# Kernel tuning notes

Measured on AMD Instinct MI355X. Metric: run time of the kernel, lower is better.

The kernel has to match this reference:

```python
import jax, jax.numpy as jnp
import numpy as np

N_HEAD = 16
D_HEAD = 64
D_MODEL = 1024
SCALE = 1.0 / D_HEAD ** 0.5


def setup_inputs() -> dict:
    key = jax.random.key(0)
    k1, k2 = jax.random.split(key)
    h = jax.random.normal(k1, (2048, 2, D_MODEL), dtype=jnp.float32)
    # torch Linear weight layout: [out_features, in_features]
    w_qkv = jax.random.normal(k2, (3 * N_HEAD * D_HEAD, D_MODEL), dtype=jnp.float32) * (D_MODEL ** -0.5)
    return {"h": h, "w_qkv": w_qkv}


def reference(h, w_qkv):
    qlen, bsz, _ = h.shape
    heads = h @ w_qkv.T  # [qlen, bsz, 3*n_head*d_head]
    head_q, head_k, head_v = jnp.split(heads, 3, axis=-1)
    head_q = head_q.reshape(qlen, bsz, N_HEAD, D_HEAD)
    head_k = head_k.reshape(qlen, bsz, N_HEAD, D_HEAD)
    head_v = head_v.reshape(qlen, bsz, N_HEAD, D_HEAD)
    attn_score = jnp.einsum('ibnd,jbnd->ijbn', head_q, head_k) * SCALE
    attn_prob = jax.nn.softmax(attn_score, axis=1)  # softmax over key dim j
    # dropout is identity at p=0.0 / eval mode
    attn_vec = jnp.einsum('ijbn,jbnd->ibnd', attn_prob, head_v)
    attn_vec = attn_vec.reshape(qlen, bsz, N_HEAD * D_HEAD)
    return attn_vec, attn_prob
```

## Files before the change

### kernel.cpp

```cpp
#include <hip/hip_runtime.h>

typedef _Float16 f16;
typedef f16 f16x8 __attribute__((ext_vector_type(8)));
typedef f16 f16x4 __attribute__((ext_vector_type(4)));
typedef float f32x4 __attribute__((ext_vector_type(4)));

#define QLEN 2048
#define BSZ 2
#define NH 16
#define DH 64
#define DM 1024
#define NBN (BSZ*NH)
#define SCALE 0.125f

static __device__ __forceinline__ f32x4 mfma16(f16x8 a, f16x8 b, f32x4 c) {
  return __builtin_amdgcn_mfma_f32_16x16x32_f16(a, b, c, 0, 0, 0);
}

static __device__ __forceinline__ void gload_lds16(const void* g, void* l) {
  __builtin_amdgcn_global_load_lds((const __attribute__((address_space(1))) unsigned int*)g,
                                   (__attribute__((address_space(3))) unsigned int*)l,
                                   16, 0, 0);
}

__global__ __launch_bounds__(256) void cvt_f32_f16(const float* __restrict__ s,
                                                   f16* __restrict__ d, int n4) {
  int idx = blockIdx.x * 256 + threadIdx.x;
  if (idx >= n4) return;
  f32x4 v = ((const f32x4*)s)[idx];
  f16x4 o;
#pragma unroll
  for (int q = 0; q < 4; ++q) o[q] = (f16)v[q];
  ((f16x4*)d)[idx] = o;
}

__global__ __launch_bounds__(256) void qkv_gemm(const f16* __restrict__ A, const f16* __restrict__ W,
                                                f16* __restrict__ Qs, f16* __restrict__ Ks,
                                                f16* __restrict__ Vt) {
  __shared__ f16 As[128 * 32];
  __shared__ f16 Bs[128 * 32];
  const int bid = blockIdx.x;
  const int r0 = (bid & 31) << 7;
  const int c0 = (bid >> 5) << 7;
  const int t = threadIdx.x;
  const int lane = t & 63, w = t >> 6;
  const int wr = (w >> 1) << 6, wc = (w & 1) << 6;
  const int l15 = lane & 15, lhi = lane >> 4;

  f32x4 acc[4][4] = {};

  const f16* ga = A + (size_t)(r0 + (t >> 2)) * DM + ((t & 3) << 3);
  const f16* gb = W + (size_t)(c0 + (t >> 2)) * DM + ((t & 3) << 3);
  char* la = (char*)As + w * 1024;
  char* lb = (char*)Bs + w * 1024;

  for (int k0 = 0; k0 < DM; k0 += 32) {
    __syncthreads();
    gload_lds16(ga + k0, la);
    gload_lds16(ga + k0 + (size_t)64 * DM, la + 4096);
    gload_lds16(gb + k0, lb);
    gload_lds16(gb + k0 + (size_t)64 * DM, lb + 4096);
    __syncthreads();
    f16x8 af[4], bf[4];
#pragma unroll
    for (int m = 0; m < 4; ++m)
      af[m] = *(const f16x8*)&As[(wr + m * 16 + l15) * 32 + lhi * 8];
#pragma unroll
    for (int n = 0; n < 4; ++n)
      bf[n] = *(const f16x8*)&Bs[(wc + n * 16 + l15) * 32 + lhi * 8];
#pragma unroll
    for (int m = 0; m < 4; ++m)
#pragma unroll
      for (int n = 0; n < 4; ++n)
        acc[m][n] = mfma16(af[m], bf[n], acc[m][n]);
  }

  const int part = c0 >> 10;
#pragma unroll
  for (int m = 0; m < 4; ++m) {
#pragma unroll
    for (int n = 0; n < 4; ++n) {
#pragma unroll
      for (int q = 0; q < 4; ++q) {
        int r = r0 + wr + m * 16 + lhi * 4 + q;
        int c = c0 + wc + n * 16 + l15;
        int i = r >> 1, b = r & 1;
        int nh = (c >> 6) & 15, d = c & 63;
        int bn = b * 16 + nh;
        f16 v = (f16)acc[m][n][q];
        if (part == 0)       Qs[((size_t)bn * QLEN + i) * DH + d] = v;
        else if (part == 1)  Ks[((size_t)bn * QLEN + i) * DH + d] = v;
        else                 Vt[((size_t)bn * DH + d) * QLEN + i] = v;
      }
    }
  }
}

__global__ __launch_bounds__(256) void flash_attn(const f16* __restrict__ Qs, const f16* __restrict__ Ks,
                                                  const f16* __restrict__ Vt, float* __restrict__ av,
                                                  float* __restrict__ sm, float* __restrict__ srl) {
  __shared__ f16 plds[4][16 * 32];
  const int bid = blockIdx.x;
  const int bn = bid >> 4, ib = bid & 15;
  const int t = threadIdx.x, lane = t & 63, w = t >> 6;
  const int l15 = lane & 15, lhi = lane >> 4;
  const int i0 = (ib << 7) + (w << 5);
  const f16* Qb = Qs + ((size_t)bn << 17);
  const f16* Kb = Ks + ((size_t)bn << 17);
  const f16* Vb = Vt + ((size_t)bn << 17);
  f16* pw = plds[w];

  f16x8 qf[2][2];
#pragma unroll
  for (int rg = 0; rg < 2; ++rg)
#pragma unroll
    for (int kc = 0; kc < 2; ++kc)
      qf[rg][kc] = *(const f16x8*)&Qb[(size_t)(i0 + rg * 16 + l15) * DH + kc * 32 + lhi * 8];

  f32x4 o[2][4] = {};
  float mrun[2][4], lrun[2][4];
#pragma unroll
  for (int rg = 0; rg < 2; ++rg)
#pragma unroll
    for (int q = 0; q < 4; ++q) { mrun[rg][q] = -1e30f; lrun[rg][q] = 0.f; }

  for (int j0 = 0; j0 < QLEN; j0 += 32) {
    f16x8 kf[2][2], vf[4];
#pragma unroll
    for (int jc = 0; jc < 2; ++jc)
#pragma unroll
      for (int kc = 0; kc < 2; ++kc)
        kf[jc][kc] = *(const f16x8*)&Kb[(size_t)(j0 + jc * 16 + l15) * DH + kc * 32 + lhi * 8];
#pragma unroll
    for (int dc = 0; dc < 4; ++dc)
      vf[dc] = *(const f16x8*)&Vb[(size_t)(dc * 16 + l15) * QLEN + j0 + lhi * 8];

#pragma unroll
    for (int rg = 0; rg < 2; ++rg) {
      f32x4 s[2];
#pragma unroll
      for (int jc = 0; jc < 2; ++jc) {
        f32x4 z = {0.f, 0.f, 0.f, 0.f};
        z = mfma16(qf[rg][0], kf[jc][0], z);
        z = mfma16(qf[rg][1], kf[jc][1], z);
        s[jc] = z;
      }
      float p[2][4], alpha[4];
#pragma unroll
      for (int q = 0; q < 4; ++q) {
        float v0 = s[0][q] * SCALE, v1 = s[1][q] * SCALE;
        float tm = fmaxf(v0, v1);
        tm = fmaxf(tm, __shfl_xor(tm, 1));
        tm = fmaxf(tm, __shfl_xor(tm, 2));
        tm = fmaxf(tm, __shfl_xor(tm, 4));
        tm = fmaxf(tm, __shfl_xor(tm, 8));
        float mnew = fmaxf(mrun[rg][q], tm);
        alpha[q] = __expf(mrun[rg][q] - mnew);
        mrun[rg][q] = mnew;
        p[0][q] = __expf(v0 - mnew);
        p[1][q] = __expf(v1 - mnew);
        float r = p[0][q] + p[1][q];
        r += __shfl_xor(r, 1);
        r += __shfl_xor(r, 2);
        r += __shfl_xor(r, 4);
        r += __shfl_xor(r, 8);
        lrun[rg][q] = lrun[rg][q] * alpha[q] + r;
      }
#pragma unroll
      for (int dc = 0; dc < 4; ++dc)
#pragma unroll
        for (int q = 0; q < 4; ++q)
          o[rg][dc][q] *= alpha[q];
#pragma unroll
      for (int jc = 0; jc < 2; ++jc)
#pragma unroll
        for (int q = 0; q < 4; ++q)
          pw[(lhi * 4 + q) * 32 + jc * 16 + l15] = (f16)p[jc][q];
      f16x8 pa = *(const f16x8*)&pw[l15 * 32 + lhi * 8];
#pragma unroll
      for (int dc = 0; dc < 4; ++dc)
        o[rg][dc] = mfma16(pa, vf[dc], o[rg][dc]);
    }
  }

  const int b = bn >> 4, nh = bn & 15;
#pragma unroll
  for (int rg = 0; rg < 2; ++rg)
#pragma unroll
    for (int dc = 0; dc < 4; ++dc)
#pragma unroll
      for (int q = 0; q < 4; ++q) {
        int i = i0 + rg * 16 + lhi * 4 + q;
        av[((size_t)i * BSZ + b) * (NH * DH) + nh * DH + dc * 16 + l15] =
            o[rg][dc][q] / lrun[rg][q];
      }
  if (l15 == 0) {
#pragma unroll
    for (int rg = 0; rg < 2; ++rg)
#pragma unroll
      for (int q = 0; q < 4; ++q) {
        int i = i0 + rg * 16 + lhi * 4 + q;
        sm[bn * QLEN + i] = mrun[rg][q];
        srl[bn * QLEN + i] = 1.0f / lrun[rg][q];
      }
  }
}

__global__ __launch_bounds__(256, 2) void write_probs(const f16* __restrict__ Qs, const f16* __restrict__ Ks,
                                                      const float* __restrict__ sm, const float* __restrict__ srl,
                                                      float* __restrict__ pout) {
  __shared__ f16 tile[2][16 * 32 * 32];
  const int bid = blockIdx.x;
  const int it = bid >> 3, jt = bid & 7;
  const int i0 = it << 4, j0 = jt << 8;
  const int t = threadIdx.x, lane = t & 63, w = t >> 6;
  const int l15 = lane & 15, lhi = lane >> 4;

  float mm[8][4], rl[8][4];
#pragma unroll
  for (int bl = 0; bl < 8; ++bl) {
    const int bn = w * 8 + bl;
#pragma unroll
    for (int q = 0; q < 4; ++q) {
      const int i = i0 + lhi * 4 + q;
      mm[bl][q] = sm[bn * QLEN + i];
      rl[bl][q] = srl[bn * QLEN + i];
    }
  }

  const int o = t & 3;
  const int jl_s = (t >> 2) & 31;
  const int ihalf = t >> 7;
  const int quad = o ^ ((jl_s & 7) >> 1);
  const bool hsw = (jl_s & 1);

  for (int ch = 0; ch < 8; ++ch) {
    f16* tb = tile[ch & 1];
    const int jbase = j0 + ch * 32;

    f16 stv[8][2][4];
#pragma unroll
    for (int bl = 0; bl < 8; ++bl) {
      const int bn = w * 8 + bl;
      const f16* Qb = Qs + ((size_t)bn << 17);
      const f16* Kb = Ks + ((size_t)bn << 17);
      f16x8 qf[2], kf[2][2];
#pragma unroll
      for (int kc = 0; kc < 2; ++kc)
        qf[kc] = *(const f16x8*)&Qb[(size_t)(i0 + l15) * DH + kc * 32 + lhi * 8];
#pragma unroll
      for (int jc = 0; jc < 2; ++jc)
#pragma unroll
        for (int kc = 0; kc < 2; ++kc)
          kf[jc][kc] = *(const f16x8*)&Kb[(size_t)(jbase + jc * 16 + l15) * DH + kc * 32 + lhi * 8];
#pragma unroll
      for (int jc = 0; jc < 2; ++jc) {
        f32x4 z = {0.f, 0.f, 0.f, 0.f};
        z = mfma16(qf[0], kf[jc][0], z);
        z = mfma16(qf[1], kf[jc][1], z);
#pragma unroll
        for (int q = 0; q < 4; ++q)
          stv[bl][jc][q] = (f16)(__expf(z[q] * SCALE - mm[bl][q]) * rl[bl][q]);
      }
    }

#pragma unroll
    for (int h = 0; h < 2; ++h) {
      const int g = w * 2 + h;
#pragma unroll
      for (int jc = 0; jc < 2; ++jc)
#pragma unroll
        for (int q = 0; q < 4; ++q) {
          const int i_l = lhi * 4 + q;
          const int jl = jc * 16 + l15;
          f16x4 v = {stv[4 * h + 0][jc][q], stv[4 * h + 1][jc][q],
                     stv[4 * h + 2][jc][q], stv[4 * h + 3][jc][q]};
          *(f16x4*)&tb[(i_l * 32 + jl) * 32 + ((g ^ (jl & 7)) << 2)] = v;
        }
    }
    __syncthreads();

#pragma unroll
    for (int p = 0; p < 8; ++p) {
      const int i_l = p * 2 + ihalf;
      f16x8 v = *(const f16x8*)&tb[(i_l * 32 + jl_s) * 32 + (quad << 3)];
      f16x4 vl = {v[0], v[1], v[2], v[3]};
      f16x4 vh = {v[4], v[5], v[6], v[7]};
      f16x4 fa = hsw ? vh : vl;
      f16x4 fb = hsw ? vl : vh;
      f32x4 lo = {(float)fa[0], (float)fa[1], (float)fa[2], (float)fa[3]};
      f32x4 hi = {(float)fb[0], (float)fb[1], (float)fb[2], (float)fb[3]};
      float* op = pout + ((size_t)(i0 + i_l) * QLEN + jbase + jl_s) * NBN + o * 8;
      __builtin_nontemporal_store(lo, (f32x4*)op);
      __builtin_nontemporal_store(hi, (f32x4*)(op + 4));
    }
  }
}

extern "C" void kernel_launch(void* const* d_in, const int* in_sizes, int n_in,
                              void* d_out, int out_size, void* d_ws, size_t ws_size,
                              hipStream_t stream) {
  const float* h  = (const float*)d_in[0];
  const float* wq = (const float*)d_in[1];
  float* av   = (float*)d_out;
  float* pout = av + (size_t)QLEN * BSZ * NH * DH;

  char* ws = (char*)d_ws;
  f16* hh  = (f16*)ws;
  f16* wh  = (f16*)(ws + (8u << 20));
  f16* Qsc = (f16*)(ws + (16u << 20));
  f16* Ksc = (f16*)(ws + (24u << 20));
  f16* Vtc = (f16*)(ws + (32u << 20));
  float* smv  = (float*)(ws + (40u << 20));
  float* srlv = (float*)(ws + (40u << 20) + (QLEN * NBN * 4));

  const int nh4 = QLEN * BSZ * DM / 4;
  const int nw4 = 3 * NH * DH * DM / 4;
  cvt_f32_f16<<<nh4 / 256, 256, 0, stream>>>(h, hh, nh4);
  cvt_f32_f16<<<nw4 / 256, 256, 0, stream>>>(wq, wh, nw4);
  qkv_gemm<<<32 * 24, 256, 0, stream>>>(hh, wh, Qsc, Ksc, Vtc);
  flash_attn<<<NBN * 16, 256, 0, stream>>>(Qsc, Ksc, Vtc, av, smv, srlv);
  write_probs<<<128 * 8, 256, 0, stream>>>(Qsc, Ksc, smv, srlv, pout);
}
```

Measured before the change: 378.8 us.

## Widen write_probs key chunk to 64 with single LDS tile and reload softmax stats

```diff
diff --git a/kernel.cpp b/kernel.cpp
--- a/kernel.cpp
+++ b/kernel.cpp
@@ -209,88 +209,82 @@
 __global__ __launch_bounds__(256, 2) void write_probs(const f16* __restrict__ Qs, const f16* __restrict__ Ks,
                                                       const float* __restrict__ sm, const float* __restrict__ srl,
                                                       float* __restrict__ pout) {
-  __shared__ f16 tile[2][16 * 32 * 32];
+  __shared__ f16 tile[16 * 64 * 32];
   const int bid = blockIdx.x;
   const int it = bid >> 3, jt = bid & 7;
   const int i0 = it << 4, j0 = jt << 8;
   const int t = threadIdx.x, lane = t & 63, w = t >> 6;
   const int l15 = lane & 15, lhi = lane >> 4;
 
-  float mm[8][4], rl[8][4];
-#pragma unroll
-  for (int bl = 0; bl < 8; ++bl) {
-    const int bn = w * 8 + bl;
-#pragma unroll
-    for (int q = 0; q < 4; ++q) {
-      const int i = i0 + lhi * 4 + q;
-      mm[bl][q] = sm[bn * QLEN + i];
-      rl[bl][q] = srl[bn * QLEN + i];
-    }
-  }
-
   const int o = t & 3;
-  const int jl_s = (t >> 2) & 31;
-  const int ihalf = t >> 7;
-  const int quad = o ^ ((jl_s & 7) >> 1);
-  const bool hsw = (jl_s & 1);
-
-  for (int ch = 0; ch < 8; ++ch) {
-    f16* tb = tile[ch & 1];
-    const int jbase = j0 + ch * 32;
-
-    f16 stv[8][2][4];
+  const int j_s = t >> 2;
+  const int sp = o ^ ((j_s & 7) >> 1);
+  const bool hsw = (j_s & 1);
+
+  for (int sc = 0; sc < 4; ++sc) {
+    const int jbase = j0 + sc * 64;
+
+    f16x4 stv[8][4];
 #pragma unroll
     for (int bl = 0; bl < 8; ++bl) {
       const int bn = w * 8 + bl;
       const f16* Qb = Qs + ((size_t)bn << 17);
       const f16* Kb = Ks + ((size_t)bn << 17);
-      f16x8 qf[2], kf[2][2];
+      f16x8 qf[2], kf[4][2];
 #pragma unroll
       for (int kc = 0; kc < 2; ++kc)
         qf[kc] = *(const f16x8*)&Qb[(size_t)(i0 + l15) * DH + kc * 32 + lhi * 8];
 #pragma unroll
-      for (int jc = 0; jc < 2; ++jc)
+      for (int jc = 0; jc < 4; ++jc)
 #pragma unroll
         for (int kc = 0; kc < 2; ++kc)
           kf[jc][kc] = *(const f16x8*)&Kb[(size_t)(jbase + jc * 16 + l15) * DH + kc * 32 + lhi * 8];
-#pragma unroll
-      for (int jc = 0; jc < 2; ++jc) {
+      float mm[4], rl[4];
+#pragma unroll
+      for (int q = 0; q < 4; ++q) {
+        const int i = i0 + lhi * 4 + q;
+        mm[q] = sm[bn * QLEN + i];
+        rl[q] = srl[bn * QLEN + i];
+      }
+#pragma unroll
+      for (int jc = 0; jc < 4; ++jc) {
         f32x4 z = {0.f, 0.f, 0.f, 0.f};
         z = mfma16(qf[0], kf[jc][0], z);
         z = mfma16(qf[1], kf[jc][1], z);
 #pragma unroll
         for (int q = 0; q < 4; ++q)
-          stv[bl][jc][q] = (f16)(__expf(z[q] * SCALE - mm[bl][q]) * rl[bl][q]);
-      }
-    }
+          stv[bl][jc][q] = (f16)(__expf(z[q] * SCALE - mm[q]) * rl[q]);
+      }
+    }
+
+    __syncthreads();
 
 #pragma unroll
     for (int h = 0; h < 2; ++h) {
       const int g = w * 2 + h;
 #pragma unroll
-      for (int jc = 0; jc < 2; ++jc)
+      for (int jc = 0; jc < 4; ++jc)
 #pragma unroll
         for (int q = 0; q < 4; ++q) {
           const int i_l = lhi * 4 + q;
           const int jl = jc * 16 + l15;
           f16x4 v = {stv[4 * h + 0][jc][q], stv[4 * h + 1][jc][q],
                      stv[4 * h + 2][jc][q], stv[4 * h + 3][jc][q]};
-          *(f16x4*)&tb[(i_l * 32 + jl) * 32 + ((g ^ (jl & 7)) << 2)] = v;
+          *(f16x4*)&tile[(i_l * 64 + jl) * 32 + ((g ^ (jl & 7)) << 2)] = v;
         }
     }
     __syncthreads();
 
 #pragma unroll
-    for (int p = 0; p < 8; ++p) {
-      const int i_l = p * 2 + ihalf;
-      f16x8 v = *(const f16x8*)&tb[(i_l * 32 + jl_s) * 32 + (quad << 3)];
+    for (int r = 0; r < 16; ++r) {
+      f16x8 v = *(const f16x8*)&tile[(r * 64 + j_s) * 32 + (sp << 3)];
       f16x4 vl = {v[0], v[1], v[2], v[3]};
       f16x4 vh = {v[4], v[5], v[6], v[7]};
       f16x4 fa = hsw ? vh : vl;
       f16x4 fb = hsw ? vl : vh;
       f32x4 lo = {(float)fa[0], (float)fa[1], (float)fa[2], (float)fa[3]};
       f32x4 hi = {(float)fb[0], (float)fb[1], (float)fb[2], (float)fb[3]};
-      float* op = pout + ((size_t)(i0 + i_l) * QLEN + jbase + jl_s) * NBN + o * 8;
+      float* op = pout + ((size_t)(i0 + r) * QLEN + jbase + j_s) * NBN + o * 8;
       __builtin_nontemporal_store(lo, (f32x4*)op);
       __builtin_nontemporal_store(hi, (f32x4*)(op + 4));
     }
```

After: 432.6 us. 14.2% more time.

## Widen QKV GEMM K-tile, swizzle LDS, and stage epilogue through LDS

Applied to the files above, without the earlier changes.

```diff
diff --git a/kernel.cpp b/kernel.cpp
--- a/kernel.cpp
+++ b/kernel.cpp
@@ -37,8 +37,9 @@
 __global__ __launch_bounds__(256) void qkv_gemm(const f16* __restrict__ A, const f16* __restrict__ W,
                                                 f16* __restrict__ Qs, f16* __restrict__ Ks,
                                                 f16* __restrict__ Vt) {
-  __shared__ f16 As[128 * 32];
-  __shared__ f16 Bs[128 * 32];
+  __shared__ f16 S[2][128 * 64];
+  f16* As = S[0];
+  f16* Bs = S[1];
   const int bid = blockIdx.x;
   const int r0 = (bid & 31) << 7;
   const int c0 = (bid >> 5) << 7;
@@ -49,50 +50,75 @@
 
   f32x4 acc[4][4] = {};
 
-  const f16* ga = A + (size_t)(r0 + (t >> 2)) * DM + ((t & 3) << 3);
-  const f16* gb = W + (size_t)(c0 + (t >> 2)) * DM + ((t & 3) << 3);
+  const int scol = (((t & 7) ^ ((t >> 3) & 7)) << 3);
+  const f16* ga = A + (size_t)(r0 + (t >> 3)) * DM + scol;
+  const f16* gb = W + (size_t)(c0 + (t >> 3)) * DM + scol;
   char* la = (char*)As + w * 1024;
   char* lb = (char*)Bs + w * 1024;
 
-  for (int k0 = 0; k0 < DM; k0 += 32) {
+  for (int k0 = 0; k0 < DM; k0 += 64) {
     __syncthreads();
-    gload_lds16(ga + k0, la);
-    gload_lds16(ga + k0 + (size_t)64 * DM, la + 4096);
-    gload_lds16(gb + k0, lb);
-    gload_lds16(gb + k0 + (size_t)64 * DM, lb + 4096);
+#pragma unroll
+    for (int it = 0; it < 4; ++it) {
+      gload_lds16(ga + k0 + (size_t)(it * 32) * DM, la + it * 4096);
+      gload_lds16(gb + k0 + (size_t)(it * 32) * DM, lb + it * 4096);
+    }
     __syncthreads();
-    f16x8 af[4], bf[4];
-#pragma unroll
-    for (int m = 0; m < 4; ++m)
-      af[m] = *(const f16x8*)&As[(wr + m * 16 + l15) * 32 + lhi * 8];
+#pragma unroll
+    for (int kk = 0; kk < 2; ++kk) {
+      f16x8 af[4], bf[4];
+#pragma unroll
+      for (int m = 0; m < 4; ++m) {
+        const int r = wr + m * 16 + l15;
+        af[m] = *(const f16x8*)&As[r * 64 + (((kk * 4 + lhi) ^ (r & 7)) << 3)];
+      }
+#pragma unroll
+      for (int n = 0; n < 4; ++n) {
+        const int r = wc + n * 16 + l15;
+        bf[n] = *(const f16x8*)&Bs[r * 64 + (((kk * 4 + lhi) ^ (r & 7)) << 3)];
+      }
+#pragma unroll
+      for (int m = 0; m < 4; ++m)
+#pragma unroll
+        for (int n = 0; n < 4; ++n)
+          acc[m][n] = mfma16(af[m], bf[n], acc[m][n]);
+    }
+  }
+
+  const int part = c0 >> 10;
+  const int nh_base = (c0 >> 6) & 15;
+  const int i0g = r0 >> 1;
+  f16* T = (f16*)S;
+
+  __syncthreads();
+#pragma unroll
+  for (int m = 0; m < 4; ++m)
 #pragma unroll
     for (int n = 0; n < 4; ++n)
-      bf[n] = *(const f16x8*)&Bs[(wc + n * 16 + l15) * 32 + lhi * 8];
-#pragma unroll
-    for (int m = 0; m < 4; ++m)
-#pragma unroll
-      for (int n = 0; n < 4; ++n)
-        acc[m][n] = mfma16(af[m], bf[n], acc[m][n]);
-  }
-
-  const int part = c0 >> 10;
-#pragma unroll
-  for (int m = 0; m < 4; ++m) {
-#pragma unroll
-    for (int n = 0; n < 4; ++n) {
 #pragma unroll
       for (int q = 0; q < 4; ++q) {
-        int r = r0 + wr + m * 16 + lhi * 4 + q;
-        int c = c0 + wc + n * 16 + l15;
-        int i = r >> 1, b = r & 1;
-        int nh = (c >> 6) & 15, d = c & 63;
-        int bn = b * 16 + nh;
-        f16 v = (f16)acc[m][n][q];
-        if (part == 0)       Qs[((size_t)bn * QLEN + i) * DH + d] = v;
-        else if (part == 1)  Ks[((size_t)bn * QLEN + i) * DH + d] = v;
-        else                 Vt[((size_t)bn * DH + d) * QLEN + i] = v;
-      }
-    }
+        const int r_l = wr + m * 16 + lhi * 4 + q;
+        const int c_l = wc + n * 16 + l15;
+        const int i_l = r_l >> 1, b = r_l & 1;
+        const int nh_l = c_l >> 6, d = c_l & 63;
+        const int bn2 = b * 2 + nh_l;
+        const f16 v = (f16)acc[m][n][q];
+        if (part < 2) T[(bn2 * 64 + i_l) * 64 + (d ^ ((i_l & 7) << 3))] = v;
+        else          T[(bn2 * 64 + d) * 64 + (i_l ^ ((d & 7) << 3))] = v;
+      }
+  __syncthreads();
+
+  {
+    const int bn2 = t >> 6, x = t & 63;
+    const int bn = (bn2 >> 1) * 16 + nh_base + (bn2 & 1);
+    f16* dst;
+    if (part == 0)      dst = Qs + ((size_t)bn * QLEN + i0g + x) * DH;
+    else if (part == 1) dst = Ks + ((size_t)bn * QLEN + i0g + x) * DH;
+    else                dst = Vt + ((size_t)bn * DH + x) * QLEN + i0g;
+    const f16* src = &T[(bn2 * 64 + x) * 64];
+#pragma unroll
+    for (int g = 0; g < 8; ++g)
+      *(f16x8*)&dst[g * 8] = *(const f16x8*)&src[(g ^ (x & 7)) << 3];
   }
 }
 
```

Result: slower. 388.0 us (+2.4%).
